# Performance work log

Hardware: AMD Instinct MI355X
Metric: run time of the kernel (lower is better)

Reference implementation:

```python
import jax, jax.numpy as jnp
import numpy as np

B, L, E, H = 2, 2048, 1024, 16
D = E // H

def setup_inputs() -> dict:
    key = jax.random.key(0)
    ks = jax.random.split(key, 6)
    values = jax.random.normal(ks[0], (B, L, E), dtype=jnp.float32)
    keys = jax.random.normal(ks[1], (B, L, E), dtype=jnp.float32)
    query = jax.random.normal(ks[2], (B, L, E), dtype=jnp.float32)
    mask = jax.random.randint(ks[3], (B, 1, L, L), 0, 2, dtype=jnp.int32)
    W_out = jax.random.normal(ks[4], (E, E), dtype=jnp.float32) * 0.02
    b_out = jax.random.normal(ks[5], (E,), dtype=jnp.float32) * 0.02
    return {"values": values, "keys": keys, "query": query, "mask": mask,
            "W_out": W_out, "b_out": b_out}

def reference(values, keys, query, mask, W_out, b_out):
    # Note: source module never applies its per-head q/k/v Linear layers;
    # it only reshapes inputs, so we do the same.
    b, l, e = query.shape
    v = values.reshape(b, l, H, D)   # [B, K, H, D]
    k = keys.reshape(b, l, H, D)     # [B, K, H, D]
    q = query.reshape(b, l, H, D)    # [B, Q, H, D]
    # scores[b,h,q,k] = sum_d q[b,q,h,d] * k[b,k,h,d]
    scores = jnp.einsum('bqhd,bkhd->bhqk', q, k)
    scores = jnp.where(mask == 0, jnp.float32(-1e20), scores)
    # source scales by 1/sqrt(embed_size), not head_dim
    attn = jax.nn.softmax(scores / jnp.float32(E ** 0.5), axis=3)
    out = jnp.einsum('bhqk,bkhd->bqhd', attn, v).reshape(b, l, e)
    out = out @ W_out.T + b_out  # torch Linear: x @ W^T + b
    return out
```

## Files before the change

### kernel.cpp

```cpp
#include <hip/hip_runtime.h>
#include <hip/hip_bf16.h>

typedef __bf16 bf16;
typedef __bf16 bf16x8 __attribute__((ext_vector_type(8)));
typedef __bf16 bf16x4 __attribute__((ext_vector_type(4)));
typedef float  f32x2  __attribute__((ext_vector_type(2)));
typedef float  f32x4  __attribute__((ext_vector_type(4)));
typedef float  f32x16 __attribute__((ext_vector_type(16)));

#define B_ 2
#define L_ 2048
#define E_ 1024
#define H_ 16
#define D_ 64

__device__ __forceinline__ int swz(int r, int c) {
    return r * 64 + (((c ^ (r & 7)) & 7) << 3);
}

#define DMA16(gp, lp)                                                              \
    __builtin_amdgcn_global_load_lds(                                              \
        (const __attribute__((address_space(1))) unsigned int*)(gp),               \
        (__attribute__((address_space(3))) unsigned int*)(lp), 16, 0, 0)

__global__ __launch_bounds__(256) void prep_kernel(const float* __restrict__ v,
                                                   const float* __restrict__ keys,
                                                   const int* __restrict__ mask,
                                                   const float* __restrict__ W,
                                                   bf16* __restrict__ vt_,
                                                   bf16* __restrict__ kt_,
                                                   unsigned int* __restrict__ mtq2,
                                                   bf16* __restrict__ wbt) {
    __shared__ __attribute__((aligned(16))) float tile[64 * 65];
    const int bid = blockIdx.x;
    const int t = threadIdx.x;
    if (bid < 1024) {
        int bh = bid >> 5, b = bh >> 4, h = bh & 15, kt = bid & 31;
        int kk = t >> 2, dg = t & 3;
        const float* src = v + (((size_t)(b * L_ + kt * 64 + kk)) * H_ + h) * D_ + dg * 16;
        float4 f[4];
#pragma unroll
        for (int i = 0; i < 4; i++) f[i] = reinterpret_cast<const float4*>(src)[i];
#pragma unroll
        for (int i = 0; i < 16; i++)
            tile[(dg * 16 + i) * 65 + kk] = reinterpret_cast<const float*>(f)[i];
        __syncthreads();
        int dd = t >> 2, cg = t & 3;
        const int sig[16] = {0, 1, 2, 3, 8, 9, 10, 11, 4, 5, 6, 7, 12, 13, 14, 15};
        bf16 tmp[16];
#pragma unroll
        for (int p = 0; p < 16; p++)
            tmp[p] = (bf16)tile[dd * 65 + cg * 16 + sig[p]];
        bf16* dst = vt_ + ((size_t)bh * 32 + kt) * 4096;
        *reinterpret_cast<uint4*>(dst + swz(dd, cg * 2))     = *reinterpret_cast<const uint4*>(&tmp[0]);
        *reinterpret_cast<uint4*>(dst + swz(dd, cg * 2 + 1)) = *reinterpret_cast<const uint4*>(&tmp[8]);
    } else if (bid < 2048) {
        int idx = bid - 1024;
        int b = idx >> 9;
        int q = (idx & 511) * 4 + (t >> 6);
        int li = t & 63;
        const int* mrow = mask + ((size_t)b * L_ + q) * L_;
        unsigned int* mq = mtq2 + (size_t)b * 64 * 2048;
#pragma unroll 2
        for (int pass = 0; pass < 8; pass++) {
            int4 m4 = reinterpret_cast<const int4*>(mrow)[pass * 64 + li];
            unsigned long long b0 = __ballot(m4.x & 1);
            unsigned long long b1 = __ballot(m4.y & 1);
            unsigned long long b2 = __ballot(m4.z & 1);
            unsigned long long b3 = __ballot(m4.w & 1);
            if (li < 8) {
                unsigned int word = (unsigned int)((b0 >> (8 * li)) & 0xFFull)
                                  | ((unsigned int)((b1 >> (8 * li)) & 0xFFull) << 8)
                                  | ((unsigned int)((b2 >> (8 * li)) & 0xFFull) << 16)
                                  | ((unsigned int)((b3 >> (8 * li)) & 0xFFull) << 24);
                mq[(size_t)(pass * 8 + li) * 2048 + q] = word;
            }
        }
    } else if (bid < 3072) {
        int idx = bid - 2048;
        int b = idx >> 9, h = (idx >> 5) & 15, kt = idx & 31;
        int r = t >> 2, cg = t & 3;
        const float* src = keys + ((size_t)(b * L_ + kt * 64 + r)) * E_ + h * 64 + cg * 16;
        float4 f[4];
#pragma unroll
        for (int i = 0; i < 4; i++) f[i] = reinterpret_cast<const float4*>(src)[i];
        bf16 tmp[16];
#pragma unroll
        for (int i = 0; i < 16; i++)
            tmp[i] = (bf16)reinterpret_cast<const float*>(f)[i];
        bf16* dst = kt_ + ((size_t)(b * 16 + h) * 32 + kt) * 4096;
        *reinterpret_cast<uint4*>(dst + swz(r, cg * 2))     = *reinterpret_cast<const uint4*>(&tmp[0]);
        *reinterpret_cast<uint4*>(dst + swz(r, cg * 2 + 1)) = *reinterpret_cast<const uint4*>(&tmp[8]);
    } else {
        int idx = bid - 3072;
        int n6 = idx >> 4, kt = idx & 15;
        int r = t >> 2, cg = t & 3;
        const float* src = W + ((size_t)(n6 * 64 + r)) * E_ + kt * 64 + cg * 16;
        float4 f[4];
#pragma unroll
        for (int i = 0; i < 4; i++) f[i] = reinterpret_cast<const float4*>(src)[i];
        bf16 tmp[16];
#pragma unroll
        for (int i = 0; i < 16; i++)
            tmp[i] = (bf16)reinterpret_cast<const float*>(f)[i];
        bf16* dst = wbt + ((size_t)(n6 * 16 + kt)) * 4096;
        *reinterpret_cast<uint4*>(dst + swz(r, cg * 2))     = *reinterpret_cast<const uint4*>(&tmp[0]);
        *reinterpret_cast<uint4*>(dst + swz(r, cg * 2 + 1)) = *reinterpret_cast<const uint4*>(&tmp[8]);
    }
}

__global__ __launch_bounds__(256, 4) void attn_kernel(const float* __restrict__ q_,
                                                      const bf16* __restrict__ kt_,
                                                      const bf16* __restrict__ vt_,
                                                      const unsigned int* __restrict__ mtq2,
                                                      bf16* __restrict__ xbt) {
    __shared__ __attribute__((aligned(16))) char smem[40960];
    bf16* Qs = (bf16*)(smem + 32768);
    float* Om = (float*)smem;
    float* Lrow = (float*)(smem + 16384);
    bf16* Xs = (bf16*)(smem + 16896);

    const int bh = blockIdx.y, b = bh >> 4, hd = bh & 15;
    const int q0 = blockIdx.x * 64;
    const int t = threadIdx.x;
    const int w = t >> 6, lane = t & 63, h = lane >> 5, l31 = lane & 31;
    const int wq = w & 1, wk = w >> 1;
    const int r_ = t >> 2, cg = t & 3;

    const float CSCALE = 1.4426950408889634f / 32.0f;

    const bf16* kbase = kt_ + (size_t)bh * 32 * 4096;
    const bf16* vbase = vt_ + (size_t)bh * 32 * 4096;

    {
        const bf16* gk = kbase + w * 1024 + lane * 8;
        DMA16(gk, smem + w * 2048);
        DMA16(gk + 512, smem + w * 2048 + 1024);
        const bf16* gv = vbase + w * 1024 + lane * 8;
        DMA16(gv, smem + 16384 + w * 2048);
        DMA16(gv + 512, smem + 16384 + w * 2048 + 1024);
    }
    {
        const float* src = q_ + ((size_t)(b * L_ + q0 + r_)) * E_ + hd * 64 + cg * 16;
        float4 f[4];
#pragma unroll
        for (int i = 0; i < 4; i++) f[i] = reinterpret_cast<const float4*>(src)[i];
        bf16 tmp[16];
#pragma unroll
        for (int i = 0; i < 16; i++)
            tmp[i] = (bf16)(reinterpret_cast<const float*>(f)[i] * CSCALE);
        *reinterpret_cast<uint4*>(&Qs[swz(r_, cg * 2)])     = *reinterpret_cast<const uint4*>(&tmp[0]);
        *reinterpret_cast<uint4*>(&Qs[swz(r_, cg * 2 + 1)]) = *reinterpret_cast<const uint4*>(&tmp[8]);
    }
    __syncthreads();

    bf16x8 bq[4];
#pragma unroll
    for (int dc = 0; dc < 4; dc++)
        bq[dc] = *reinterpret_cast<const bf16x8*>(&Qs[swz(wq * 32 + l31, dc * 2 + h)]);

    f32x16 oc[2] = {{}, {}};
    f32x2 ls = {0.0f, 0.0f};

    const unsigned int* mbase = mtq2 + (size_t)b * 64 * 2048 + q0 + wq * 32 + l31;
    unsigned int mw = mbase[(size_t)wk * 2048];

    for (int kt = 0; kt < L_ / 64; kt++) {
        __syncthreads();
        bf16* Kc = (bf16*)(smem + (kt & 1) * 8192);
        bf16* Vc = (bf16*)(smem + 16384 + (kt & 1) * 8192);
        if (kt + 1 < L_ / 64) {
            char* Kn = smem + ((kt + 1) & 1) * 8192;
            char* Vn = smem + 16384 + ((kt + 1) & 1) * 8192;
            const bf16* gk = kbase + (size_t)(kt + 1) * 4096 + w * 1024 + lane * 8;
            DMA16(gk, Kn + w * 2048);
            DMA16(gk + 512, Kn + w * 2048 + 1024);
            const bf16* gv = vbase + (size_t)(kt + 1) * 4096 + w * 1024 + lane * 8;
            DMA16(gv, Vn + w * 2048);
            DMA16(gv + 512, Vn + w * 2048 + 1024);
        }
        unsigned int mw_nxt = (kt + 1 < L_ / 64)
                                  ? mbase[(size_t)((kt + 1) * 2 + wk) * 2048] : 0u;

        f32x16 st = {};
        __builtin_amdgcn_s_setprio(1);
#pragma unroll
        for (int dc = 0; dc < 4; dc++) {
            bf16x8 ak = *reinterpret_cast<const bf16x8*>(&Kc[swz(wk * 32 + l31, dc * 2 + h)]);
            st = __builtin_amdgcn_mfma_f32_32x32x16_bf16(ak, bq[dc], st, 0, 0, 0);
        }
        __builtin_amdgcn_s_setprio(0);

        const unsigned int mwh = mw >> h;
        float pv[16];
#pragma unroll
        for (int i = 0; i < 16; i += 2) {
            const int b0 = 8 * (i & 3) + 2 * (i >> 2);
            const int b1 = 8 * ((i + 1) & 3) + 2 * ((i + 1) >> 2);
            float e0 = __builtin_amdgcn_exp2f(st[i]);
            float e1 = __builtin_amdgcn_exp2f(st[i + 1]);
            int m0 = ((int)(mwh << (31 - b0))) >> 31;
            int m1 = ((int)(mwh << (31 - b1))) >> 31;
            pv[i]     = __int_as_float(__float_as_int(e0) & m0);
            pv[i + 1] = __int_as_float(__float_as_int(e1) & m1);
            ls += (f32x2){pv[i], pv[i + 1]};
        }
        bf16x8 bp[2];
#pragma unroll
        for (int kc = 0; kc < 2; kc++)
#pragma unroll
            for (int j = 0; j < 8; j++)
                bp[kc][j] = (bf16)pv[kc * 8 + j];

        __builtin_amdgcn_s_setprio(1);
#pragma unroll
        for (int da = 0; da < 2; da++)
#pragma unroll
            for (int kc = 0; kc < 2; kc++) {
                bf16x8 av = *reinterpret_cast<const bf16x8*>(&Vc[swz(da * 32 + l31, wk * 4 + kc * 2 + h)]);
                oc[da] = __builtin_amdgcn_mfma_f32_32x32x16_bf16(av, bp[kc], oc[da], 0, 0, 0);
            }
        __builtin_amdgcn_s_setprio(0);
        mw = mw_nxt;
    }
    __syncthreads();

    float lsum = ls.x + ls.y;
    float lw = lsum + __shfl(lsum, lane ^ 32, 64);
    if (wk == 1) {
#pragma unroll
        for (int da = 0; da < 2; da++)
#pragma unroll
            for (int i = 0; i < 16; i++) {
                int d = da * 32 + (i & 3) + 8 * (i >> 2) + 4 * h;
                Om[d * 64 + wq * 32 + l31] = oc[da][i];
            }
        if (h == 0) Lrow[wq * 32 + l31] = lw;
    }
    __syncthreads();
    if (wk == 0) {
        float rinv = 1.0f / (lw + Lrow[wq * 32 + l31]);
#pragma unroll
        for (int da = 0; da < 2; da++)
#pragma unroll
            for (int g = 0; g < 4; g++) {
                int d0 = da * 32 + 8 * g + 4 * h;
                bf16x4 pk;
#pragma unroll
                for (int r = 0; r < 4; r++)
                    pk[r] = (bf16)((oc[da][g * 4 + r] + Om[(d0 + r) * 64 + wq * 32 + l31]) * rinv);
                *reinterpret_cast<bf16x4*>(&Xs[(wq * 32 + l31) * 72 + d0]) = pk;
            }
    }
    __syncthreads();
    {
        bf16* xtile = xbt + ((size_t)((b * 32 + (q0 >> 6)) * 16 + hd)) * 4096;
        *reinterpret_cast<uint4*>(xtile + swz(r_, cg * 2))     = *reinterpret_cast<const uint4*>(&Xs[r_ * 72 + cg * 16]);
        *reinterpret_cast<uint4*>(xtile + swz(r_, cg * 2 + 1)) = *reinterpret_cast<const uint4*>(&Xs[r_ * 72 + cg * 16 + 8]);
    }
}

__global__ __launch_bounds__(256, 3) void proj_kernel(const bf16* __restrict__ xbt,
                                                      const bf16* __restrict__ wbt,
                                                      const float* __restrict__ bias,
                                                      float* __restrict__ out) {
    __shared__ __attribute__((aligned(16))) char smem[49152];
    const int n0 = blockIdx.x * 64, m0 = blockIdx.y * 128;
    const int t = threadIdx.x;
    const int w = t >> 6, lane = t & 63, h = lane >> 5, l31 = lane & 31;
    const int wm = w >> 1, wn = w & 1;

    const bf16* a0 = xbt + ((size_t)(m0 >> 6)) * 16 * 4096;
    const bf16* a1 = a0 + 16 * 4096;
    const bf16* bb_ = wbt + ((size_t)(n0 >> 6)) * 16 * 4096;

    {
#pragma unroll
        for (int i = 0; i < 4; i++) {
            int c = w * 4 + i;
            const bf16* g = ((c >> 3) ? a1 : a0) + (c & 7) * 512 + lane * 8;
            DMA16(g, smem + c * 1024);
        }
#pragma unroll
        for (int i = 0; i < 2; i++) {
            int c = w * 2 + i;
            DMA16(bb_ + c * 512 + lane * 8, smem + 32768 + c * 1024);
        }
    }

    f32x16 acc[2] = {{}, {}};
    for (int kt = 0; kt < E_ / 64; kt++) {
        __syncthreads();
        bf16* Ac = (bf16*)(smem + (kt & 1) * 16384);
        bf16* Bc = (bf16*)(smem + 32768 + (kt & 1) * 8192);
        if (kt + 1 < E_ / 64) {
            char* An = smem + ((kt + 1) & 1) * 16384;
            char* Bn = smem + 32768 + ((kt + 1) & 1) * 8192;
            const bf16* an0 = a0 + (kt + 1) * 4096;
            const bf16* an1 = a1 + (kt + 1) * 4096;
            const bf16* bn = bb_ + (kt + 1) * 4096;
#pragma unroll
            for (int i = 0; i < 4; i++) {
                int c = w * 4 + i;
                const bf16* g = ((c >> 3) ? an1 : an0) + (c & 7) * 512 + lane * 8;
                DMA16(g, An + c * 1024);
            }
#pragma unroll
            for (int i = 0; i < 2; i++) {
                int c = w * 2 + i;
                DMA16(bn + c * 512 + lane * 8, Bn + c * 1024);
            }
        }
#pragma unroll
        for (int dc = 0; dc < 4; dc++) {
            bf16x8 bfr = *reinterpret_cast<const bf16x8*>(&Bc[swz(wn * 32 + l31, dc * 2 + h)]);
#pragma unroll
            for (int mi = 0; mi < 2; mi++) {
                bf16x8 afr = *reinterpret_cast<const bf16x8*>(&Ac[wm * 4096 + swz(mi * 32 + l31, dc * 2 + h)]);
                acc[mi] = __builtin_amdgcn_mfma_f32_32x32x16_bf16(afr, bfr, acc[mi], 0, 0, 0);
            }
        }
    }

    float bv = bias[n0 + wn * 32 + l31];
#pragma unroll
    for (int mi = 0; mi < 2; mi++)
#pragma unroll
        for (int i = 0; i < 16; i++) {
            int row = m0 + wm * 64 + mi * 32 + (i & 3) + 8 * (i >> 2) + 4 * h;
            out[(size_t)row * E_ + n0 + wn * 32 + l31] = acc[mi][i] + bv;
        }
}

extern "C" void kernel_launch(void* const* d_in, const int* in_sizes, int n_in,
                              void* d_out, int out_size, void* d_ws, size_t ws_size,
                              hipStream_t stream) {
    (void)in_sizes; (void)n_in; (void)out_size; (void)ws_size;
    const float* values = (const float*)d_in[0];
    const float* keys   = (const float*)d_in[1];
    const float* query  = (const float*)d_in[2];
    const int*   mask   = (const int*)d_in[3];
    const float* W_out  = (const float*)d_in[4];
    const float* b_out  = (const float*)d_in[5];
    float* out = (float*)d_out;

    char* ws = (char*)d_ws;
    bf16* vt_ = (bf16*)(ws);
    bf16* kt_ = (bf16*)(ws + 8388608);
    bf16* wbt = (bf16*)(ws + 16777216);
    unsigned int* mtq2 = (unsigned int*)(ws + 18874368);
    bf16* xbt = (bf16*)(ws + 19922944);

    prep_kernel<<<3328, 256, 0, stream>>>(values, keys, mask, W_out, vt_, kt_, mtq2, wbt);
    attn_kernel<<<dim3(L_ / 64, B_ * H_), 256, 0, stream>>>(query, kt_, vt_, mtq2, xbt);
    proj_kernel<<<dim3(E_ / 64, (B_ * L_) / 128), 256, 0, stream>>>(xbt, wbt, b_out, out);
}
```

Measured before the change: 191.6 us.

## Split fused prep kernel into four kernels and stage mask bits through LDS

Splits the branchy fused prep kernel into separate V-transpose, mask-pack, K-convert and W-convert kernels. The mask packer is restructured so each block handles a 64-query by 256-key tile, gathers the packed words in shared memory, and writes them out as coalesced rows instead of scattered 4-byte stores. Splitting removes per-block branching and lets each kernel use only the shared memory it needs, at the cost of three extra launches that run one after another.

```diff
diff --git a/kernel.cpp b/kernel.cpp
--- a/kernel.cpp
+++ b/kernel.cpp
@@ -23,90 +23,102 @@
         (const __attribute__((address_space(1))) unsigned int*)(gp),               \
         (__attribute__((address_space(3))) unsigned int*)(lp), 16, 0, 0)
 
-__global__ __launch_bounds__(256) void prep_kernel(const float* __restrict__ v,
-                                                   const float* __restrict__ keys,
-                                                   const int* __restrict__ mask,
-                                                   const float* __restrict__ W,
-                                                   bf16* __restrict__ vt_,
-                                                   bf16* __restrict__ kt_,
-                                                   unsigned int* __restrict__ mtq2,
-                                                   bf16* __restrict__ wbt) {
+
+__global__ __launch_bounds__(256) void prep_v(const float* __restrict__ v,
+                                              bf16* __restrict__ vt_) {
     __shared__ __attribute__((aligned(16))) float tile[64 * 65];
     const int bid = blockIdx.x;
     const int t = threadIdx.x;
-    if (bid < 1024) {
-        int bh = bid >> 5, b = bh >> 4, h = bh & 15, kt = bid & 31;
-        int kk = t >> 2, dg = t & 3;
-        const float* src = v + (((size_t)(b * L_ + kt * 64 + kk)) * H_ + h) * D_ + dg * 16;
-        float4 f[4];
-#pragma unroll
-        for (int i = 0; i < 4; i++) f[i] = reinterpret_cast<const float4*>(src)[i];
-#pragma unroll
-        for (int i = 0; i < 16; i++)
-            tile[(dg * 16 + i) * 65 + kk] = reinterpret_cast<const float*>(f)[i];
-        __syncthreads();
-        int dd = t >> 2, cg = t & 3;
-        const int sig[16] = {0, 1, 2, 3, 8, 9, 10, 11, 4, 5, 6, 7, 12, 13, 14, 15};
-        bf16 tmp[16];
-#pragma unroll
-        for (int p = 0; p < 16; p++)
-            tmp[p] = (bf16)tile[dd * 65 + cg * 16 + sig[p]];
-        bf16* dst = vt_ + ((size_t)bh * 32 + kt) * 4096;
-        *reinterpret_cast<uint4*>(dst + swz(dd, cg * 2))     = *reinterpret_cast<const uint4*>(&tmp[0]);
-        *reinterpret_cast<uint4*>(dst + swz(dd, cg * 2 + 1)) = *reinterpret_cast<const uint4*>(&tmp[8]);
-    } else if (bid < 2048) {
-        int idx = bid - 1024;
-        int b = idx >> 9;
-        int q = (idx & 511) * 4 + (t >> 6);
-        int li = t & 63;
-        const int* mrow = mask + ((size_t)b * L_ + q) * L_;
-        unsigned int* mq = mtq2 + (size_t)b * 64 * 2048;
-#pragma unroll 2
-        for (int pass = 0; pass < 8; pass++) {
-            int4 m4 = reinterpret_cast<const int4*>(mrow)[pass * 64 + li];
-            unsigned long long b0 = __ballot(m4.x & 1);
-            unsigned long long b1 = __ballot(m4.y & 1);
-            unsigned long long b2 = __ballot(m4.z & 1);
-            unsigned long long b3 = __ballot(m4.w & 1);
-            if (li < 8) {
-                unsigned int word = (unsigned int)((b0 >> (8 * li)) & 0xFFull)
-                                  | ((unsigned int)((b1 >> (8 * li)) & 0xFFull) << 8)
-                                  | ((unsigned int)((b2 >> (8 * li)) & 0xFFull) << 16)
-                                  | ((unsigned int)((b3 >> (8 * li)) & 0xFFull) << 24);
-                mq[(size_t)(pass * 8 + li) * 2048 + q] = word;
-            }
-        }
-    } else if (bid < 3072) {
-        int idx = bid - 2048;
-        int b = idx >> 9, h = (idx >> 5) & 15, kt = idx & 31;
-        int r = t >> 2, cg = t & 3;
-        const float* src = keys + ((size_t)(b * L_ + kt * 64 + r)) * E_ + h * 64 + cg * 16;
-        float4 f[4];
-#pragma unroll
-        for (int i = 0; i < 4; i++) f[i] = reinterpret_cast<const float4*>(src)[i];
-        bf16 tmp[16];
-#pragma unroll
-        for (int i = 0; i < 16; i++)
-            tmp[i] = (bf16)reinterpret_cast<const float*>(f)[i];
-        bf16* dst = kt_ + ((size_t)(b * 16 + h) * 32 + kt) * 4096;
-        *reinterpret_cast<uint4*>(dst + swz(r, cg * 2))     = *reinterpret_cast<const uint4*>(&tmp[0]);
-        *reinterpret_cast<uint4*>(dst + swz(r, cg * 2 + 1)) = *reinterpret_cast<const uint4*>(&tmp[8]);
-    } else {
-        int idx = bid - 3072;
-        int n6 = idx >> 4, kt = idx & 15;
-        int r = t >> 2, cg = t & 3;
-        const float* src = W + ((size_t)(n6 * 64 + r)) * E_ + kt * 64 + cg * 16;
-        float4 f[4];
-#pragma unroll
-        for (int i = 0; i < 4; i++) f[i] = reinterpret_cast<const float4*>(src)[i];
-        bf16 tmp[16];
-#pragma unroll
-        for (int i = 0; i < 16; i++)
-            tmp[i] = (bf16)reinterpret_cast<const float*>(f)[i];
-        bf16* dst = wbt + ((size_t)(n6 * 16 + kt)) * 4096;
-        *reinterpret_cast<uint4*>(dst + swz(r, cg * 2))     = *reinterpret_cast<const uint4*>(&tmp[0]);
-        *reinterpret_cast<uint4*>(dst + swz(r, cg * 2 + 1)) = *reinterpret_cast<const uint4*>(&tmp[8]);
-    }
+    int bh = bid >> 5, b = bh >> 4, h = bh & 15, kt = bid & 31;
+    int kk = t >> 2, dg = t & 3;
+    const float* src = v + (((size_t)(b * L_ + kt * 64 + kk)) * H_ + h) * D_ + dg * 16;
+    float4 f[4];
+#pragma unroll
+    for (int i = 0; i < 4; i++) f[i] = reinterpret_cast<const float4*>(src)[i];
+#pragma unroll
+    for (int i = 0; i < 16; i++)
+        tile[(dg * 16 + i) * 65 + kk] = reinterpret_cast<const float*>(f)[i];
+    __syncthreads();
+    int dd = t >> 2, cg = t & 3;
+    const int sig[16] = {0, 1, 2, 3, 8, 9, 10, 11, 4, 5, 6, 7, 12, 13, 14, 15};
+    bf16 tmp[16];
+#pragma unroll
+    for (int p = 0; p < 16; p++)
+        tmp[p] = (bf16)tile[dd * 65 + cg * 16 + sig[p]];
+    bf16* dst = vt_ + ((size_t)bh * 32 + kt) * 4096;
+    *reinterpret_cast<uint4*>(dst + swz(dd, cg * 2))     = *reinterpret_cast<const uint4*>(&tmp[0]);
+    *reinterpret_cast<uint4*>(dst + swz(dd, cg * 2 + 1)) = *reinterpret_cast<const uint4*>(&tmp[8]);
+}
+
+__global__ __launch_bounds__(256) void prep_mask(const int* __restrict__ mask,
+                                                 unsigned int* __restrict__ mtq2) {
+    __shared__ unsigned int wq[8][65];
+    const int bid = blockIdx.x;
+    const int kc = bid & 7;
+    const int qt = (bid >> 3) & 31;
+    const int b  = bid >> 8;
+    const int t = threadIdx.x;
+    const int w = t >> 6, li = t & 63;
+    const int q0 = qt * 64;
+    const int* mbase = mask + ((size_t)b * L_ + q0) * L_ + kc * 256;
+#pragma unroll 4
+    for (int i = 0; i < 16; i++) {
+        int q = w * 16 + i;
+        int4 m4 = reinterpret_cast<const int4*>(mbase + (size_t)q * L_)[li];
+        unsigned long long b0 = __ballot(m4.x & 1);
+        unsigned long long b1 = __ballot(m4.y & 1);
+        unsigned long long b2 = __ballot(m4.z & 1);
+        unsigned long long b3 = __ballot(m4.w & 1);
+        if (li < 8) {
+            unsigned int word = (unsigned int)((b0 >> (8 * li)) & 0xFFull)
+                              | ((unsigned int)((b1 >> (8 * li)) & 0xFFull) << 8)
+                              | ((unsigned int)((b2 >> (8 * li)) & 0xFFull) << 16)
+                              | ((unsigned int)((b3 >> (8 * li)) & 0xFFull) << 24);
+            wq[li][q] = word;
+        }
+    }
+    __syncthreads();
+    unsigned int* mq = mtq2 + (size_t)b * 64 * 2048 + q0;
+    mq[(size_t)(kc * 8 + w) * 2048 + li]     = wq[w][li];
+    mq[(size_t)(kc * 8 + w + 4) * 2048 + li] = wq[w + 4][li];
+}
+
+__global__ __launch_bounds__(256) void prep_k(const float* __restrict__ keys,
+                                              bf16* __restrict__ kt_) {
+    const int bid = blockIdx.x;
+    const int t = threadIdx.x;
+    int b = bid >> 9, h = (bid >> 5) & 15, kt = bid & 31;
+    int r = t >> 2, cg = t & 3;
+    const float* src = keys + ((size_t)(b * L_ + kt * 64 + r)) * E_ + h * 64 + cg * 16;
+    float4 f[4];
+#pragma unroll
+    for (int i = 0; i < 4; i++) f[i] = reinterpret_cast<const float4*>(src)[i];
+    bf16 tmp[16];
+#pragma unroll
+    for (int i = 0; i < 16; i++)
+        tmp[i] = (bf16)reinterpret_cast<const float*>(f)[i];
+    bf16* dst = kt_ + ((size_t)(b * 16 + h) * 32 + kt) * 4096;
+    *reinterpret_cast<uint4*>(dst + swz(r, cg * 2))     = *reinterpret_cast<const uint4*>(&tmp[0]);
+    *reinterpret_cast<uint4*>(dst + swz(r, cg * 2 + 1)) = *reinterpret_cast<const uint4*>(&tmp[8]);
+}
+
+__global__ __launch_bounds__(256) void prep_w(const float* __restrict__ W,
+                                              bf16* __restrict__ wbt) {
+    const int bid = blockIdx.x;
+    const int t = threadIdx.x;
+    int n6 = bid >> 4, kt = bid & 15;
+    int r = t >> 2, cg = t & 3;
+    const float* src = W + ((size_t)(n6 * 64 + r)) * E_ + kt * 64 + cg * 16;
+    float4 f[4];
+#pragma unroll
+    for (int i = 0; i < 4; i++) f[i] = reinterpret_cast<const float4*>(src)[i];
+    bf16 tmp[16];
+#pragma unroll
+    for (int i = 0; i < 16; i++)
+        tmp[i] = (bf16)reinterpret_cast<const float*>(f)[i];
+    bf16* dst = wbt + ((size_t)(n6 * 16 + kt)) * 4096;
+    *reinterpret_cast<uint4*>(dst + swz(r, cg * 2))     = *reinterpret_cast<const uint4*>(&tmp[0]);
+    *reinterpret_cast<uint4*>(dst + swz(r, cg * 2 + 1)) = *reinterpret_cast<const uint4*>(&tmp[8]);
 }
 
 __global__ __launch_bounds__(256, 4) void attn_kernel(const float* __restrict__ q_,
@@ -351,7 +363,10 @@
     unsigned int* mtq2 = (unsigned int*)(ws + 18874368);
     bf16* xbt = (bf16*)(ws + 19922944);
 
-    prep_kernel<<<3328, 256, 0, stream>>>(values, keys, mask, W_out, vt_, kt_, mtq2, wbt);
+    prep_v<<<1024, 256, 0, stream>>>(values, vt_);
+    prep_mask<<<512, 256, 0, stream>>>(mask, mtq2);
+    prep_k<<<1024, 256, 0, stream>>>(keys, kt_);
+    prep_w<<<256, 256, 0, stream>>>(W_out, wbt);
     attn_kernel<<<dim3(L_ / 64, B_ * H_), 256, 0, stream>>>(query, kt_, vt_, mtq2, xbt);
     proj_kernel<<<dim3(E_ / 64, (B_ * L_) / 128), 256, 0, stream>>>(xbt, wbt, b_out, out);
 }
```

Result: slower. 205.1 us (+7.0%).

## Halve attention query tile and read K/V directly from global memory

Applied to the files above, without the earlier changes.

The attention kernel now processes 32 query rows per block instead of 64, so it launches twice as many blocks. Each of the four waves takes a disjoint quarter of the key tiles and loads its K/V fragments straight from global memory (via cache) rather than through double-buffered LDS DMA with per-tile barriers. The partial outputs and row sums from the four waves are then reduced serially through shared memory. This cuts LDS use and barriers to raise occupancy and remove per-iteration synchronization, at the cost of redundant K/V global/L2 traffic, since reuse across query rows within a block is lost, and a longer epilogue reduction.

```diff
diff --git a/kernel.cpp b/kernel.cpp
--- a/kernel.cpp
+++ b/kernel.cpp
@@ -5,7 +5,6 @@
 typedef __bf16 bf16x8 __attribute__((ext_vector_type(8)));
 typedef __bf16 bf16x4 __attribute__((ext_vector_type(4)));
 typedef float  f32x2  __attribute__((ext_vector_type(2)));
-typedef float  f32x4  __attribute__((ext_vector_type(4)));
 typedef float  f32x16 __attribute__((ext_vector_type(16)));
 
 #define B_ 2
@@ -109,23 +108,21 @@
     }
 }
 
-__global__ __launch_bounds__(256, 4) void attn_kernel(const float* __restrict__ q_,
+__global__ __launch_bounds__(256, 5) void attn_kernel(const float* __restrict__ q_,
                                                       const bf16* __restrict__ kt_,
                                                       const bf16* __restrict__ vt_,
                                                       const unsigned int* __restrict__ mtq2,
                                                       bf16* __restrict__ xbt) {
-    __shared__ __attribute__((aligned(16))) char smem[40960];
-    bf16* Qs = (bf16*)(smem + 32768);
+    __shared__ __attribute__((aligned(16))) char smem[13312];
+    bf16* Qs = (bf16*)smem;
     float* Om = (float*)smem;
-    float* Lrow = (float*)(smem + 16384);
-    bf16* Xs = (bf16*)(smem + 16896);
+    float* Lsum = (float*)(smem + 8192);
+    bf16* Xs = (bf16*)(smem + 8704);
 
     const int bh = blockIdx.y, b = bh >> 4, hd = bh & 15;
-    const int q0 = blockIdx.x * 64;
+    const int q0 = blockIdx.x * 32;
     const int t = threadIdx.x;
-    const int w = t >> 6, lane = t & 63, h = lane >> 5, l31 = lane & 31;
-    const int wq = w & 1, wk = w >> 1;
-    const int r_ = t >> 2, cg = t & 3;
+    const int wk = t >> 6, lane = t & 63, h = lane >> 5, l31 = lane & 31;
 
     const float CSCALE = 1.4426950408889634f / 32.0f;
 
@@ -133,77 +130,79 @@
     const bf16* vbase = vt_ + (size_t)bh * 32 * 4096;
 
     {
-        const bf16* gk = kbase + w * 1024 + lane * 8;
-        DMA16(gk, smem + w * 2048);
-        DMA16(gk + 512, smem + w * 2048 + 1024);
-        const bf16* gv = vbase + w * 1024 + lane * 8;
-        DMA16(gv, smem + 16384 + w * 2048);
-        DMA16(gv + 512, smem + 16384 + w * 2048 + 1024);
-    }
-    {
-        const float* src = q_ + ((size_t)(b * L_ + q0 + r_)) * E_ + hd * 64 + cg * 16;
-        float4 f[4];
-#pragma unroll
-        for (int i = 0; i < 4; i++) f[i] = reinterpret_cast<const float4*>(src)[i];
-        bf16 tmp[16];
-#pragma unroll
-        for (int i = 0; i < 16; i++)
-            tmp[i] = (bf16)(reinterpret_cast<const float*>(f)[i] * CSCALE);
-        *reinterpret_cast<uint4*>(&Qs[swz(r_, cg * 2)])     = *reinterpret_cast<const uint4*>(&tmp[0]);
-        *reinterpret_cast<uint4*>(&Qs[swz(r_, cg * 2 + 1)]) = *reinterpret_cast<const uint4*>(&tmp[8]);
+        const int r = t >> 3, c8 = t & 7;
+        const float* src = q_ + ((size_t)(b * L_ + q0 + r)) * E_ + hd * 64 + c8 * 8;
+        float4 f0 = reinterpret_cast<const float4*>(src)[0];
+        float4 f1 = reinterpret_cast<const float4*>(src)[1];
+        bf16 tmp[8];
+        tmp[0] = (bf16)(f0.x * CSCALE); tmp[1] = (bf16)(f0.y * CSCALE);
+        tmp[2] = (bf16)(f0.z * CSCALE); tmp[3] = (bf16)(f0.w * CSCALE);
+        tmp[4] = (bf16)(f1.x * CSCALE); tmp[5] = (bf16)(f1.y * CSCALE);
+        tmp[6] = (bf16)(f1.z * CSCALE); tmp[7] = (bf16)(f1.w * CSCALE);
+        *reinterpret_cast<uint4*>(&Qs[swz(r, c8)]) = *reinterpret_cast<const uint4*>(&tmp[0]);
     }
     __syncthreads();
 
     bf16x8 bq[4];
 #pragma unroll
     for (int dc = 0; dc < 4; dc++)
-        bq[dc] = *reinterpret_cast<const bf16x8*>(&Qs[swz(wq * 32 + l31, dc * 2 + h)]);
+        bq[dc] = *reinterpret_cast<const bf16x8*>(&Qs[swz(l31, dc * 2 + h)]);
+    __syncthreads();
+
+    const int kh = (wk & 1) * 32;
+    int cK[4], cV[4];
+#pragma unroll
+    for (int dc = 0; dc < 4; dc++)
+        cK[dc] = swz(kh + l31, dc * 2 + h);
+#pragma unroll
+    for (int j = 0; j < 4; j++) {
+        const int da = j >> 1, kc = j & 1;
+        cV[j] = swz(da * 32 + l31, (wk & 1) * 4 + kc * 2 + h);
+    }
 
     f32x16 oc[2] = {{}, {}};
     f32x2 ls = {0.0f, 0.0f};
 
-    const unsigned int* mbase = mtq2 + (size_t)b * 64 * 2048 + q0 + wq * 32 + l31;
+    const unsigned int* mbase = mtq2 + (size_t)b * 64 * 2048 + q0 + l31;
     unsigned int mw = mbase[(size_t)wk * 2048];
-
-    for (int kt = 0; kt < L_ / 64; kt++) {
-        __syncthreads();
-        bf16* Kc = (bf16*)(smem + (kt & 1) * 8192);
-        bf16* Vc = (bf16*)(smem + 16384 + (kt & 1) * 8192);
-        if (kt + 1 < L_ / 64) {
-            char* Kn = smem + ((kt + 1) & 1) * 8192;
-            char* Vn = smem + 16384 + ((kt + 1) & 1) * 8192;
-            const bf16* gk = kbase + (size_t)(kt + 1) * 4096 + w * 1024 + lane * 8;
-            DMA16(gk, Kn + w * 2048);
-            DMA16(gk + 512, Kn + w * 2048 + 1024);
-            const bf16* gv = vbase + (size_t)(kt + 1) * 4096 + w * 1024 + lane * 8;
-            DMA16(gv, Vn + w * 2048);
-            DMA16(gv + 512, Vn + w * 2048 + 1024);
-        }
-        unsigned int mw_nxt = (kt + 1 < L_ / 64)
-                                  ? mbase[(size_t)((kt + 1) * 2 + wk) * 2048] : 0u;
+    int toff = (wk >> 1) * 4096;
+
+#pragma unroll 1
+    for (int i = 0; i < 16; i++) {
+        unsigned int mw_nxt = 0;
+        if (i + 1 < 16) mw_nxt = mbase[(size_t)(wk + 4 * (i + 1)) * 2048];
+
+        bf16x8 ak0 = *reinterpret_cast<const bf16x8*>(kbase + toff + cK[0]);
+        bf16x8 ak1 = *reinterpret_cast<const bf16x8*>(kbase + toff + cK[1]);
+        bf16x8 ak2 = *reinterpret_cast<const bf16x8*>(kbase + toff + cK[2]);
+        bf16x8 ak3 = *reinterpret_cast<const bf16x8*>(kbase + toff + cK[3]);
 
         f32x16 st = {};
         __builtin_amdgcn_s_setprio(1);
-#pragma unroll
-        for (int dc = 0; dc < 4; dc++) {
-            bf16x8 ak = *reinterpret_cast<const bf16x8*>(&Kc[swz(wk * 32 + l31, dc * 2 + h)]);
-            st = __builtin_amdgcn_mfma_f32_32x32x16_bf16(ak, bq[dc], st, 0, 0, 0);
-        }
+        st = __builtin_amdgcn_mfma_f32_32x32x16_bf16(ak0, bq[0], st, 0, 0, 0);
+        st = __builtin_amdgcn_mfma_f32_32x32x16_bf16(ak1, bq[1], st, 0, 0, 0);
+        st = __builtin_amdgcn_mfma_f32_32x32x16_bf16(ak2, bq[2], st, 0, 0, 0);
+        st = __builtin_amdgcn_mfma_f32_32x32x16_bf16(ak3, bq[3], st, 0, 0, 0);
         __builtin_amdgcn_s_setprio(0);
+
+        bf16x8 av0 = *reinterpret_cast<const bf16x8*>(vbase + toff + cV[0]);
+        bf16x8 av1 = *reinterpret_cast<const bf16x8*>(vbase + toff + cV[1]);
+        bf16x8 av2 = *reinterpret_cast<const bf16x8*>(vbase + toff + cV[2]);
+        bf16x8 av3 = *reinterpret_cast<const bf16x8*>(vbase + toff + cV[3]);
 
         const unsigned int mwh = mw >> h;
         float pv[16];
 #pragma unroll
-        for (int i = 0; i < 16; i += 2) {
-            const int b0 = 8 * (i & 3) + 2 * (i >> 2);
-            const int b1 = 8 * ((i + 1) & 3) + 2 * ((i + 1) >> 2);
-            float e0 = __builtin_amdgcn_exp2f(st[i]);
-            float e1 = __builtin_amdgcn_exp2f(st[i + 1]);
+        for (int e = 0; e < 16; e += 2) {
+            const int b0 = 8 * (e & 3) + 2 * (e >> 2);
+            const int b1 = 8 * ((e + 1) & 3) + 2 * ((e + 1) >> 2);
+            float e0 = __builtin_amdgcn_exp2f(st[e]);
+            float e1 = __builtin_amdgcn_exp2f(st[e + 1]);
             int m0 = ((int)(mwh << (31 - b0))) >> 31;
             int m1 = ((int)(mwh << (31 - b1))) >> 31;
-            pv[i]     = __int_as_float(__float_as_int(e0) & m0);
-            pv[i + 1] = __int_as_float(__float_as_int(e1) & m1);
-            ls += (f32x2){pv[i], pv[i + 1]};
+            pv[e]     = __int_as_float(__float_as_int(e0) & m0);
+            pv[e + 1] = __int_as_float(__float_as_int(e1) & m1);
+            ls += (f32x2){pv[e], pv[e + 1]};
         }
         bf16x8 bp[2];
 #pragma unroll
@@ -213,33 +212,52 @@
                 bp[kc][j] = (bf16)pv[kc * 8 + j];
 
         __builtin_amdgcn_s_setprio(1);
-#pragma unroll
-        for (int da = 0; da < 2; da++)
-#pragma unroll
-            for (int kc = 0; kc < 2; kc++) {
-                bf16x8 av = *reinterpret_cast<const bf16x8*>(&Vc[swz(da * 32 + l31, wk * 4 + kc * 2 + h)]);
-                oc[da] = __builtin_amdgcn_mfma_f32_32x32x16_bf16(av, bp[kc], oc[da], 0, 0, 0);
-            }
+        oc[0] = __builtin_amdgcn_mfma_f32_32x32x16_bf16(av0, bp[0], oc[0], 0, 0, 0);
+        oc[0] = __builtin_amdgcn_mfma_f32_32x32x16_bf16(av1, bp[1], oc[0], 0, 0, 0);
+        oc[1] = __builtin_amdgcn_mfma_f32_32x32x16_bf16(av2, bp[0], oc[1], 0, 0, 0);
+        oc[1] = __builtin_amdgcn_mfma_f32_32x32x16_bf16(av3, bp[1], oc[1], 0, 0, 0);
         __builtin_amdgcn_s_setprio(0);
+
+        toff += 8192;
         mw = mw_nxt;
     }
-    __syncthreads();
 
     float lsum = ls.x + ls.y;
     float lw = lsum + __shfl(lsum, lane ^ 32, 64);
+    if (h == 0) Lsum[wk * 32 + l31] = lw;
+    if (wk == 3) {
+#pragma unroll
+        for (int da = 0; da < 2; da++)
+#pragma unroll
+            for (int e = 0; e < 16; e++) {
+                int d = da * 32 + (e & 3) + 8 * (e >> 2) + 4 * h;
+                Om[d * 32 + l31] = oc[da][e];
+            }
+    }
+    __syncthreads();
+    if (wk == 2) {
+#pragma unroll
+        for (int da = 0; da < 2; da++)
+#pragma unroll
+            for (int e = 0; e < 16; e++) {
+                int d = da * 32 + (e & 3) + 8 * (e >> 2) + 4 * h;
+                Om[d * 32 + l31] += oc[da][e];
+            }
+    }
+    __syncthreads();
     if (wk == 1) {
 #pragma unroll
         for (int da = 0; da < 2; da++)
 #pragma unroll
-            for (int i = 0; i < 16; i++) {
-                int d = da * 32 + (i & 3) + 8 * (i >> 2) + 4 * h;
-                Om[d * 64 + wq * 32 + l31] = oc[da][i];
-            }
-        if (h == 0) Lrow[wq * 32 + l31] = lw;
+            for (int e = 0; e < 16; e++) {
+                int d = da * 32 + (e & 3) + 8 * (e >> 2) + 4 * h;
+                Om[d * 32 + l31] += oc[da][e];
+            }
     }
     __syncthreads();
     if (wk == 0) {
-        float rinv = 1.0f / (lw + Lrow[wq * 32 + l31]);
+        float denom = Lsum[l31] + Lsum[32 + l31] + Lsum[64 + l31] + Lsum[96 + l31];
+        float rinv = 1.0f / denom;
 #pragma unroll
         for (int da = 0; da < 2; da++)
 #pragma unroll
@@ -248,15 +266,16 @@
                 bf16x4 pk;
 #pragma unroll
                 for (int r = 0; r < 4; r++)
-                    pk[r] = (bf16)((oc[da][g * 4 + r] + Om[(d0 + r) * 64 + wq * 32 + l31]) * rinv);
-                *reinterpret_cast<bf16x4*>(&Xs[(wq * 32 + l31) * 72 + d0]) = pk;
+                    pk[r] = (bf16)((oc[da][g * 4 + r] + Om[(d0 + r) * 32 + l31]) * rinv);
+                *reinterpret_cast<bf16x4*>(&Xs[l31 * 72 + d0]) = pk;
             }
     }
     __syncthreads();
     {
+        const int r2 = t >> 3, c8 = t & 7;
         bf16* xtile = xbt + ((size_t)((b * 32 + (q0 >> 6)) * 16 + hd)) * 4096;
-        *reinterpret_cast<uint4*>(xtile + swz(r_, cg * 2))     = *reinterpret_cast<const uint4*>(&Xs[r_ * 72 + cg * 16]);
-        *reinterpret_cast<uint4*>(xtile + swz(r_, cg * 2 + 1)) = *reinterpret_cast<const uint4*>(&Xs[r_ * 72 + cg * 16 + 8]);
+        *reinterpret_cast<uint4*>(xtile + swz((blockIdx.x & 1) * 32 + r2, c8)) =
+            *reinterpret_cast<const uint4*>(&Xs[r2 * 72 + c8 * 8]);
     }
 }
 
@@ -352,6 +371,6 @@
     bf16* xbt = (bf16*)(ws + 19922944);
 
     prep_kernel<<<3328, 256, 0, stream>>>(values, keys, mask, W_out, vt_, kt_, mtq2, wbt);
-    attn_kernel<<<dim3(L_ / 64, B_ * H_), 256, 0, stream>>>(query, kt_, vt_, mtq2, xbt);
+    attn_kernel<<<dim3(L_ / 32, B_ * H_), 256, 0, stream>>>(query, kt_, vt_, mtq2, xbt);
     proj_kernel<<<dim3(E_ / 64, (B_ * L_) / 128), 256, 0, stream>>>(xbt, wbt, b_out, out);
 }
```

After: 279.3 us. 45.7% more time.
